# Optimization experiments

Measured on AMD Instinct MI355X. Metric: run time of the kernel, lower is better.

## Reference

```python
import jax, jax.numpy as jnp
import numpy as np

B, S, D, H = 2, 2048, 512, 8
DK = D // H
DECAY = 0.02
LN_EPS = 1e-5


def setup_inputs() -> dict:
    key = jax.random.key(0)
    ks = jax.random.split(key, 16)
    sd = 1.0 / np.sqrt(D)
    def lin(k, fan_in, fan_out):
        return jax.random.uniform(k, (fan_in, fan_out), jnp.float32, -sd, sd)
    return {
        "x": jax.random.normal(ks[0], (B, S, D), jnp.float32),
        "wq": lin(ks[1], D, D), "bq": jnp.zeros((D,), jnp.float32),
        "wk": lin(ks[2], D, D), "bk": jnp.zeros((D,), jnp.float32),
        "wv": lin(ks[3], D, D), "bv": jnp.zeros((D,), jnp.float32),
        "wo": lin(ks[4], D, D), "bo": jnp.zeros((D,), jnp.float32),
        "g1_w": lin(ks[5], D, D // 2), "g1_b": jnp.zeros((D // 2,), jnp.float32),
        "g2_w": lin(ks[6], D // 2, 1), "g2_b": jnp.zeros((1,), jnp.float32),
        "ln_g": jnp.ones((D,), jnp.float32), "ln_b": jnp.zeros((D,), jnp.float32),
    }


def _temporal_bias(seq_len):
    # exp(-decay * |i-j|) masked to lower triangle (causal), additive bias
    pos = jnp.arange(seq_len)
    dist = jnp.abs(pos[:, None] - pos[None, :]).astype(jnp.float32)
    bias = jnp.exp(-DECAY * dist)
    return jnp.tril(bias)  # (S, S)


def reference(x, wq, bq, wk, bk, wv, bv, wo, bo, g1_w, g1_b, g2_w, g2_b, ln_g, ln_b):
    b, s, d = x.shape
    # projections -> (B, H, S, DK)
    q = (x @ wq + bq).reshape(b, s, H, DK).transpose(0, 2, 1, 3)
    k = (x @ wk + bk).reshape(b, s, H, DK).transpose(0, 2, 1, 3)
    v = (x @ wv + bv).reshape(b, s, H, DK).transpose(0, 2, 1, 3)
    scores = jnp.einsum("bhqd,bhkd->bhqk", q, k) / jnp.sqrt(jnp.float32(DK))
    scores = scores + _temporal_bias(s)[None, None, :, :]
    attn = jax.nn.softmax(scores, axis=-1)  # (B, H, S, S)
    out = jnp.einsum("bhqk,bhkd->bhqd", attn, v)
    out = out.transpose(0, 2, 1, 3).reshape(b, s, d)
    out = out @ wo + bo
    # gated residual
    gate = jax.nn.sigmoid(jax.nn.relu(x @ g1_w + g1_b) @ g2_w + g2_b)  # (B, S, 1)
    out = out * gate + x * (1.0 - gate)
    # layer norm
    mu = jnp.mean(out, axis=-1, keepdims=True)
    var = jnp.var(out, axis=-1, keepdims=True)
    y = (out - mu) / jnp.sqrt(var + LN_EPS) * ln_g + ln_b
    return (y, attn)
```

## Files before the change

### kernel.cpp

```cpp
#include <hip/hip_runtime.h>

#define BB 2
#define SS 2048
#define DD 512
#define HH 8
#define DKK 64
#define NROWS (BB * SS)
#define Y_SIZE (BB * SS * DD)

typedef __attribute__((ext_vector_type(8))) short short8;
typedef __attribute__((ext_vector_type(4))) float f32x4;

__device__ __forceinline__ ushort f2bf(float f) {
  union { float f; unsigned u; } v; v.f = f;
  unsigned u = v.u;
  return (ushort)((u + 0x7fffu + ((u >> 16) & 1u)) >> 16);
}


__global__ __launch_bounds__(256) void conv_x_kernel(const float* __restrict__ x,
                                                     ushort* __restrict__ xb) {
  int i = (blockIdx.x * 256 + threadIdx.x) * 4;
  float4 v = *(const float4*)(x + i);
  ushort4 o = {f2bf(v.x), f2bf(v.y), f2bf(v.z), f2bf(v.w)};
  *(ushort4*)(xb + i) = o;
}

__global__ __launch_bounds__(256) void conv_wt_kernel(
    const float* __restrict__ w0, const float* __restrict__ w1,
    const float* __restrict__ w2, const float* __restrict__ w3,
    ushort* __restrict__ o0, ushort* __restrict__ o1,
    ushort* __restrict__ o2, ushort* __restrict__ o3) {
  __shared__ float T[64][65];
  const float* w; ushort* wt;
  switch (blockIdx.z) {
    case 0: w = w0; wt = o0; break;
    case 1: w = w1; wt = o1; break;
    case 2: w = w2; wt = o2; break;
    default: w = w3; wt = o3; break;
  }
  const int t = threadIdx.x;
  const int n0 = blockIdx.x * 64, k0 = blockIdx.y * 64;
#pragma unroll
  for (int i = 0; i < 4; ++i) {
    int c = t + i * 256;
    int row = c >> 4, cc = c & 15;
    float4 v = *(const float4*)(w + (size_t)(k0 + row) * DD + n0 + cc * 4);
    T[row][cc * 4 + 0] = v.x; T[row][cc * 4 + 1] = v.y;
    T[row][cc * 4 + 2] = v.z; T[row][cc * 4 + 3] = v.w;
  }
  __syncthreads();
#pragma unroll
  for (int i = 0; i < 2; ++i) {
    int c = t + i * 256;
    int nr = c >> 3, kc = c & 7;
    ushort4 a, b;
    a.x = f2bf(T[kc * 8 + 0][nr]); a.y = f2bf(T[kc * 8 + 1][nr]);
    a.z = f2bf(T[kc * 8 + 2][nr]); a.w = f2bf(T[kc * 8 + 3][nr]);
    b.x = f2bf(T[kc * 8 + 4][nr]); b.y = f2bf(T[kc * 8 + 5][nr]);
    b.z = f2bf(T[kc * 8 + 6][nr]); b.w = f2bf(T[kc * 8 + 7][nr]);
    *(ushort4*)(wt + (size_t)(n0 + nr) * DD + k0 + kc * 8) = a;
    *(ushort4*)(wt + (size_t)(n0 + nr) * DD + k0 + kc * 8 + 4) = b;
  }
}


__device__ __forceinline__ void mfma_gemm64(
    const ushort* __restrict__ A, int lda, const ushort* __restrict__ B, int ldb,
    int K, ushort (*As)[72], ushort (*Bs)[72], f32x4 (&acc)[2][2], int t) {
  const int l = t & 63, w = t >> 6;
  const int mq = w & 1, nq = w >> 1;
  const int l15 = l & 15, l4 = l >> 4;
  for (int k0 = 0; k0 < K; k0 += 64) {
    __syncthreads();
#pragma unroll
    for (int i = 0; i < 2; ++i) {
      int c = t + i * 256;
      int row = c >> 3, cc = c & 7;
      *(uint4*)&As[row][cc * 8] = *(const uint4*)(A + (size_t)row * lda + k0 + cc * 8);
      *(uint4*)&Bs[row][cc * 8] = *(const uint4*)(B + (size_t)row * ldb + k0 + cc * 8);
    }
    __syncthreads();
    short8 af[2][2], bf[2][2];
#pragma unroll
    for (int mt = 0; mt < 2; ++mt)
#pragma unroll
      for (int ks = 0; ks < 2; ++ks)
        af[mt][ks] = *(const short8*)&As[32 * mq + 16 * mt + l15][ks * 32 + l4 * 8];
#pragma unroll
    for (int nt = 0; nt < 2; ++nt)
#pragma unroll
      for (int ks = 0; ks < 2; ++ks)
        bf[nt][ks] = *(const short8*)&Bs[32 * nq + 16 * nt + l15][ks * 32 + l4 * 8];
#pragma unroll
    for (int mt = 0; mt < 2; ++mt)
#pragma unroll
      for (int nt = 0; nt < 2; ++nt)
#pragma unroll
        for (int ks = 0; ks < 2; ++ks)
          acc[mt][nt] = __builtin_amdgcn_mfma_f32_16x16x32_bf16(
              af[mt][ks], bf[nt][ks], acc[mt][nt], 0, 0, 0);
  }
}


__global__ __launch_bounds__(256) void proj_qkv_kernel(
    const ushort* __restrict__ xb,
    const ushort* __restrict__ wqt, const float* __restrict__ bq,
    const ushort* __restrict__ wkt, const float* __restrict__ bk,
    const ushort* __restrict__ wvt, const float* __restrict__ bv,
    ushort* __restrict__ qb, ushort* __restrict__ kb, ushort* __restrict__ vt) {
  __shared__ ushort As[64][72], Bs[64][72];
  const ushort* W; const float* bias; ushort* out;
  if (blockIdx.z == 0) { W = wqt; bias = bq; out = qb; }
  else if (blockIdx.z == 1) { W = wkt; bias = bk; out = kb; }
  else { W = wvt; bias = bv; out = vt; }
  const int m0 = blockIdx.x * 64;
  const int h = blockIdx.y;
  const int t = threadIdx.x;
  const int l = t & 63, w = t >> 6;
  const int mq = w & 1, nq = w >> 1;
  const int l15 = l & 15, l4 = l >> 4;
  f32x4 acc[2][2] = {};
  mfma_gemm64(xb + (size_t)m0 * DD, DD, W + (size_t)h * DKK * DD, DD, DD,
              As, Bs, acc, t);
  float biasv[2];
#pragma unroll
  for (int nt = 0; nt < 2; ++nt) biasv[nt] = bias[h * DKK + 32 * nq + 16 * nt + l15];

  if (blockIdx.z < 2) {
    __syncthreads();
#pragma unroll
    for (int mt = 0; mt < 2; ++mt)
#pragma unroll
      for (int nt = 0; nt < 2; ++nt)
#pragma unroll
        for (int r = 0; r < 4; ++r)
          As[32 * mq + 16 * mt + l4 * 4 + r][32 * nq + 16 * nt + l15] =
              f2bf(acc[mt][nt][r] + biasv[nt]);
    __syncthreads();
#pragma unroll
    for (int i = 0; i < 2; ++i) {
      int c = t + i * 256;
      int row = c >> 3, cc = c & 7;
      int m = m0 + row, b = m >> 11, s = m & (SS - 1);
      uint4 v = *(const uint4*)&As[row][cc * 8];
      *(uint4*)(out + ((size_t)(b * HH + h) * SS + s) * DKK + cc * 8) = v;
    }
  } else {
#pragma unroll
    for (int mt = 0; mt < 2; ++mt)
#pragma unroll
      for (int nt = 0; nt < 2; ++nt) {
        int dk = 32 * nq + 16 * nt + l15;
        int m = m0 + 32 * mq + 16 * mt + l4 * 4;
        int b = m >> 11, sb = m & (SS - 1);
        ushort4 pk;
        pk.x = f2bf(acc[mt][nt][0] + biasv[nt]);
        pk.y = f2bf(acc[mt][nt][1] + biasv[nt]);
        pk.z = f2bf(acc[mt][nt][2] + biasv[nt]);
        pk.w = f2bf(acc[mt][nt][3] + biasv[nt]);
        *(ushort4*)(out + ((size_t)(b * HH + h) * DKK + dk) * SS + sb) = pk;
      }
  }
}


__global__ __launch_bounds__(256) void attn_kernel(
    const ushort* __restrict__ qb, const ushort* __restrict__ kb,
    const ushort* __restrict__ vt, float* __restrict__ attn,
    ushort* __restrict__ ctx) {
  __shared__ ushort Ks[64][72], Vs[64][72], Ps[64][72];
  __shared__ float rs[64];
  const int t = threadIdx.x;
  const int l = t & 63, w = t >> 6;
  const int mq = w & 1, nq = w >> 1;
  const int l15 = l & 15, l4 = l >> 4;
  const int z = blockIdx.y;
  const int q0 = blockIdx.x * 64;
  if (t < 64) rs[t] = 0.f;

  short8 qf[2][2];
#pragma unroll
  for (int mt = 0; mt < 2; ++mt)
#pragma unroll
    for (int ks = 0; ks < 2; ++ks)
      qf[mt][ks] = *(const short8*)(qb +
          ((size_t)z * SS + q0 + 32 * mq + 16 * mt + l15) * DKK + ks * 32 + l4 * 8);

  float rowf[2][4]; int qi_[2][4];
#pragma unroll
  for (int mt = 0; mt < 2; ++mt)
#pragma unroll
    for (int r = 0; r < 4; ++r) {
      int qi = q0 + 32 * mq + 16 * mt + l4 * 4 + r;
      qi_[mt][r] = qi;
      rowf[mt][r] = __expf(-0.02f * (float)qi);
    }

  float rsp[2][4] = {};
  for (int kt = 0; kt < 32; ++kt) {
    __syncthreads();
#pragma unroll
    for (int i = 0; i < 2; ++i) {
      int c = t + i * 256;
      int row = c >> 3, cc = c & 7;
      *(uint4*)&Ks[row][cc * 8] =
          *(const uint4*)(kb + ((size_t)z * SS + kt * 64 + row) * DKK + cc * 8);
    }
    __syncthreads();
    short8 bf[2][2];
#pragma unroll
    for (int nt = 0; nt < 2; ++nt)
#pragma unroll
      for (int ks = 0; ks < 2; ++ks)
        bf[nt][ks] = *(const short8*)&Ks[32 * nq + 16 * nt + l15][ks * 32 + l4 * 8];
    f32x4 acc[2][2] = {};
#pragma unroll
    for (int mt = 0; mt < 2; ++mt)
#pragma unroll
      for (int nt = 0; nt < 2; ++nt)
#pragma unroll
        for (int ks = 0; ks < 2; ++ks)
          acc[mt][nt] = __builtin_amdgcn_mfma_f32_16x16x32_bf16(
              qf[mt][ks], bf[nt][ks], acc[mt][nt], 0, 0, 0);
#pragma unroll
    for (int nt = 0; nt < 2; ++nt) {
      int kj = kt * 64 + 32 * nq + 16 * nt + l15;
      float colf = __expf(0.02f * (float)kj);
#pragma unroll
      for (int mt = 0; mt < 2; ++mt)
#pragma unroll
        for (int r = 0; r < 4; ++r) {
          float bias = (kj <= qi_[mt][r]) ? rowf[mt][r] * colf : 0.f;
          rsp[mt][r] += __expf(fmaf(acc[mt][nt][r], 0.125f, bias));
        }
    }
  }
#pragma unroll
  for (int mt = 0; mt < 2; ++mt)
#pragma unroll
    for (int r = 0; r < 4; ++r) {
      float v = rsp[mt][r];
      v += __shfl_xor(v, 1); v += __shfl_xor(v, 2);
      v += __shfl_xor(v, 4); v += __shfl_xor(v, 8);
      if (l15 == 0) atomicAdd(&rs[32 * mq + 16 * mt + l4 * 4 + r], v);
    }
  __syncthreads();
  float inv[2][4];
#pragma unroll
  for (int mt = 0; mt < 2; ++mt)
#pragma unroll
    for (int r = 0; r < 4; ++r)
      inv[mt][r] = 1.f / rs[32 * mq + 16 * mt + l4 * 4 + r];

  f32x4 oacc[2][2] = {};
  for (int kt = 0; kt < 32; ++kt) {
    __syncthreads();
#pragma unroll
    for (int i = 0; i < 2; ++i) {
      int c = t + i * 256;
      int row = c >> 3, cc = c & 7;
      *(uint4*)&Ks[row][cc * 8] =
          *(const uint4*)(kb + ((size_t)z * SS + kt * 64 + row) * DKK + cc * 8);
      *(uint4*)&Vs[row][cc * 8] =
          *(const uint4*)(vt + ((size_t)z * DKK + row) * SS + kt * 64 + cc * 8);
    }
    __syncthreads();
    short8 bf[2][2];
#pragma unroll
    for (int nt = 0; nt < 2; ++nt)
#pragma unroll
      for (int ks = 0; ks < 2; ++ks)
        bf[nt][ks] = *(const short8*)&Ks[32 * nq + 16 * nt + l15][ks * 32 + l4 * 8];
    f32x4 acc[2][2] = {};
#pragma unroll
    for (int mt = 0; mt < 2; ++mt)
#pragma unroll
      for (int nt = 0; nt < 2; ++nt)
#pragma unroll
        for (int ks = 0; ks < 2; ++ks)
          acc[mt][nt] = __builtin_amdgcn_mfma_f32_16x16x32_bf16(
              qf[mt][ks], bf[nt][ks], acc[mt][nt], 0, 0, 0);
#pragma unroll
    for (int nt = 0; nt < 2; ++nt) {
      int kj = kt * 64 + 32 * nq + 16 * nt + l15;
      float colf = __expf(0.02f * (float)kj);
#pragma unroll
      for (int mt = 0; mt < 2; ++mt)
#pragma unroll
        for (int r = 0; r < 4; ++r) {
          float bias = (kj <= qi_[mt][r]) ? rowf[mt][r] * colf : 0.f;
          float p = __expf(fmaf(acc[mt][nt][r], 0.125f, bias)) * inv[mt][r];
          attn[((size_t)z * SS + qi_[mt][r]) * SS + kj] = p;
          Ps[32 * mq + 16 * mt + l4 * 4 + r][32 * nq + 16 * nt + l15] = f2bf(p);
        }
    }
    __syncthreads();
    short8 pa[2][2], pb[2][2];
#pragma unroll
    for (int mt = 0; mt < 2; ++mt)
#pragma unroll
      for (int ks = 0; ks < 2; ++ks)
        pa[mt][ks] = *(const short8*)&Ps[32 * mq + 16 * mt + l15][ks * 32 + l4 * 8];
#pragma unroll
    for (int nt = 0; nt < 2; ++nt)
#pragma unroll
      for (int ks = 0; ks < 2; ++ks)
        pb[nt][ks] = *(const short8*)&Vs[32 * nq + 16 * nt + l15][ks * 32 + l4 * 8];
#pragma unroll
    for (int mt = 0; mt < 2; ++mt)
#pragma unroll
      for (int nt = 0; nt < 2; ++nt)
#pragma unroll
        for (int ks = 0; ks < 2; ++ks)
          oacc[mt][nt] = __builtin_amdgcn_mfma_f32_16x16x32_bf16(
              pa[mt][ks], pb[nt][ks], oacc[mt][nt], 0, 0, 0);
  }
  __syncthreads();
#pragma unroll
  for (int mt = 0; mt < 2; ++mt)
#pragma unroll
    for (int nt = 0; nt < 2; ++nt)
#pragma unroll
      for (int r = 0; r < 4; ++r)
        Ps[32 * mq + 16 * mt + l4 * 4 + r][32 * nq + 16 * nt + l15] =
            f2bf(oacc[mt][nt][r]);
  __syncthreads();
  const int b = z >> 3, h = z & 7;
#pragma unroll
  for (int i = 0; i < 2; ++i) {
    int c = t + i * 256;
    int row = c >> 3, cc = c & 7;
    uint4 v = *(const uint4*)&Ps[row][cc * 8];
    *(uint4*)(ctx + ((size_t)(b * SS + q0 + row)) * DD + h * DKK + cc * 8) = v;
  }
}


__global__ __launch_bounds__(256) void proj_o_kernel(
    const ushort* __restrict__ ctx, const ushort* __restrict__ wot,
    const float* __restrict__ bo, float* __restrict__ o) {
  __shared__ ushort As[64][72], Bs[64][72];
  const int m0 = blockIdx.x * 64, n0 = blockIdx.y * 64;
  const int t = threadIdx.x;
  const int l = t & 63, w = t >> 6;
  const int mq = w & 1, nq = w >> 1;
  const int l15 = l & 15, l4 = l >> 4;
  f32x4 acc[2][2] = {};
  mfma_gemm64(ctx + (size_t)m0 * DD, DD, wot + (size_t)n0 * DD, DD, DD,
              As, Bs, acc, t);
#pragma unroll
  for (int nt = 0; nt < 2; ++nt) {
    int col = n0 + 32 * nq + 16 * nt + l15;
    float bv = bo[col];
#pragma unroll
    for (int mt = 0; mt < 2; ++mt)
#pragma unroll
      for (int r = 0; r < 4; ++r) {
        int m = m0 + 32 * mq + 16 * mt + l4 * 4 + r;
        o[(size_t)m * DD + col] = acc[mt][nt][r] + bv;
      }
  }
}


__global__ __launch_bounds__(256) void gate_kernel(
    const float* __restrict__ x, const float* __restrict__ g1w,
    const float* __restrict__ g1b, const float* __restrict__ g2w,
    const float* __restrict__ g2b, float* __restrict__ gate) {
  __shared__ float xs[8][512];
  __shared__ float red[32];
  const int r0 = blockIdx.x * 8;
  const int t = threadIdx.x;
  const float4* xg = (const float4*)&x[(size_t)r0 * DD];
  float4* xsv = (float4*)&xs[0][0];
#pragma unroll
  for (int i = 0; i < 4; ++i) xsv[t + i * 256] = xg[t + i * 256];
  __syncthreads();
  float acc[8] = {};
  for (int i = 0; i < 512; i += 4) {
    float w0 = g1w[(i + 0) * 256 + t];
    float w1 = g1w[(i + 1) * 256 + t];
    float w2 = g1w[(i + 2) * 256 + t];
    float w3 = g1w[(i + 3) * 256 + t];
#pragma unroll
    for (int r = 0; r < 8; ++r) {
      float4 xv = *(const float4*)&xs[r][i];
      acc[r] += xv.x * w0 + xv.y * w1 + xv.z * w2 + xv.w * w3;
    }
  }
  float b1 = g1b[t], w2_ = g2w[t];
  float p[8];
#pragma unroll
  for (int r = 0; r < 8; ++r) {
    float h = acc[r] + b1;
    h = h > 0.f ? h : 0.f;
    p[r] = h * w2_;
  }
#pragma unroll
  for (int r = 0; r < 8; ++r)
    for (int off = 32; off; off >>= 1) p[r] += __shfl_xor(p[r], off, 64);
  if ((t & 63) == 0) {
#pragma unroll
    for (int r = 0; r < 8; ++r) red[r * 4 + (t >> 6)] = p[r];
  }
  __syncthreads();
  if (t < 8) {
    float s = red[t * 4] + red[t * 4 + 1] + red[t * 4 + 2] + red[t * 4 + 3] + g2b[0];
    gate[r0 + t] = 1.f / (1.f + __expf(-s));
  }
}


__global__ __launch_bounds__(256) void blend_ln_kernel(
    const float* __restrict__ o, const float* __restrict__ x,
    const float* __restrict__ gate, const float* __restrict__ ln_g,
    const float* __restrict__ ln_b, float* __restrict__ y) {
  __shared__ float r1[4], r2[4];
  const int row = blockIdx.x, t = threadIdx.x;
  float g = gate[row];
  float2 o2 = *(const float2*)&o[(size_t)row * DD + t * 2];
  float2 x2 = *(const float2*)&x[(size_t)row * DD + t * 2];
  float va = o2.x * g + x2.x * (1.f - g);
  float vb = o2.y * g + x2.y * (1.f - g);
  float s = va + vb, q = va * va + vb * vb;
  for (int off = 32; off; off >>= 1) {
    s += __shfl_xor(s, off, 64);
    q += __shfl_xor(q, off, 64);
  }
  if ((t & 63) == 0) { r1[t >> 6] = s; r2[t >> 6] = q; }
  __syncthreads();
  s = r1[0] + r1[1] + r1[2] + r1[3];
  q = r2[0] + r2[1] + r2[2] + r2[3];
  float mean = s * (1.f / 512.f);
  float var = q * (1.f / 512.f) - mean * mean;
  float rstd = rsqrtf(var + 1e-5f);
  float2 lg = *(const float2*)&ln_g[t * 2];
  float2 lb = *(const float2*)&ln_b[t * 2];
  float2 out;
  out.x = (va - mean) * rstd * lg.x + lb.x;
  out.y = (vb - mean) * rstd * lg.y + lb.y;
  *(float2*)&y[(size_t)row * DD + t * 2] = out;
}

extern "C" void kernel_launch(void* const* d_in, const int* in_sizes, int n_in,
                              void* d_out, int out_size, void* d_ws, size_t ws_size,
                              hipStream_t stream) {
  const float* x   = (const float*)d_in[0];
  const float* wq  = (const float*)d_in[1];
  const float* bq  = (const float*)d_in[2];
  const float* wk  = (const float*)d_in[3];
  const float* bk  = (const float*)d_in[4];
  const float* wv  = (const float*)d_in[5];
  const float* bv  = (const float*)d_in[6];
  const float* wo  = (const float*)d_in[7];
  const float* bo  = (const float*)d_in[8];
  const float* g1w = (const float*)d_in[9];
  const float* g1b = (const float*)d_in[10];
  const float* g2w = (const float*)d_in[11];
  const float* g2b = (const float*)d_in[12];
  const float* lng = (const float*)d_in[13];
  const float* lnb = (const float*)d_in[14];

  float* y    = (float*)d_out;
  float* attn = y + (size_t)Y_SIZE;

  char* ws = (char*)d_ws;
  ushort* xb  = (ushort*)(ws);
  ushort* wqt = (ushort*)(ws + (4 << 20));
  ushort* wkt = (ushort*)(ws + (4 << 20) + (512 << 10));
  ushort* wvt = (ushort*)(ws + (5 << 20));
  ushort* wot = (ushort*)(ws + (5 << 20) + (512 << 10));
  ushort* qb  = (ushort*)(ws + (6 << 20));
  ushort* kb  = (ushort*)(ws + (10 << 20));
  ushort* vt  = (ushort*)(ws + (14 << 20));
  ushort* ctx = (ushort*)(ws + (18 << 20));
  float*  o   = (float*)(ws + (22 << 20));
  float*  gate= (float*)(ws + (30 << 20));

  hipLaunchKernelGGL(conv_x_kernel, dim3(Y_SIZE / 1024), dim3(256), 0, stream, x, xb);
  hipLaunchKernelGGL(conv_wt_kernel, dim3(8, 8, 4), dim3(256), 0, stream,
                     wq, wk, wv, wo, wqt, wkt, wvt, wot);
  hipLaunchKernelGGL(proj_qkv_kernel, dim3(64, 8, 3), dim3(256), 0, stream,
                     xb, wqt, bq, wkt, bk, wvt, bv, qb, kb, vt);
  hipLaunchKernelGGL(gate_kernel, dim3(512), dim3(256), 0, stream,
                     x, g1w, g1b, g2w, g2b, gate);
  hipLaunchKernelGGL(attn_kernel, dim3(32, 16), dim3(256), 0, stream,
                     qb, kb, vt, attn, ctx);
  hipLaunchKernelGGL(proj_o_kernel, dim3(64, 8), dim3(256), 0, stream,
                     ctx, wot, bo, o);
  hipLaunchKernelGGL(blend_ln_kernel, dim3(4096), dim3(256), 0, stream,
                     o, x, gate, lng, lnb, y);
}
```

Before: 446.3 us.

## Double-buffer attention tiles via register prefetch with 512-thread blocks

Rewrites the attention kernel to use 512-thread blocks that process 128-key tiles. The next K/V tile is prefetched into registers while the current tile is computed, which is meant to hide global-load latency behind MFMA and softmax work. It also raises wave priority around the MFMA blocks, uses explicit barriers and waitcnt in place of __syncthreads, and swaps the grid order so blocks of the same head are adjacent. In exchange it increases register pressure and LDS footprint and needs careful manual synchronisation.

```diff
diff --git a/kernel.cpp b/kernel.cpp
--- a/kernel.cpp
+++ b/kernel.cpp
@@ -166,18 +166,26 @@
 }
 
 
-__global__ __launch_bounds__(256) void attn_kernel(
+#define LGKM0() do { asm volatile("s_waitcnt lgkmcnt(0)" ::: "memory"); \
+                     __builtin_amdgcn_sched_barrier(0); } while (0)
+#define BARRIER() do { __builtin_amdgcn_sched_barrier(0); \
+                       __builtin_amdgcn_s_barrier(); \
+                       __builtin_amdgcn_sched_barrier(0); } while (0)
+
+__global__ __launch_bounds__(512, 2) void attn_kernel(
     const ushort* __restrict__ qb, const ushort* __restrict__ kb,
     const ushort* __restrict__ vt, float* __restrict__ attn,
     ushort* __restrict__ ctx) {
-  __shared__ ushort Ks[64][72], Vs[64][72], Ps[64][72];
+  __shared__ __align__(16) ushort Ks[128][72];
+  __shared__ __align__(16) ushort Vs[64][136];
+  __shared__ __align__(16) ushort Ps[64][136];
   __shared__ float rs[64];
   const int t = threadIdx.x;
   const int l = t & 63, w = t >> 6;
   const int mq = w & 1, nq = w >> 1;
   const int l15 = l & 15, l4 = l >> 4;
-  const int z = blockIdx.y;
-  const int q0 = blockIdx.x * 64;
+  const int z = blockIdx.x;
+  const int q0 = blockIdx.y * 64;
   if (t < 64) rs[t] = 0.f;
 
   short8 qf[2][2];
@@ -198,24 +206,46 @@
       rowf[mt][r] = __expf(-0.02f * (float)qi);
     }
 
+  uint4 kr[2], vr[2];
+  const int krow = t >> 3, kcol = (t & 7) * 8;
+  const int krow2 = krow + 64;
+  const int vrow = t >> 4, vcol = (t & 15) * 8;
+  const int vrow2 = vrow + 32;
+
+  auto kload = [&](int kt2) {
+    const ushort* p = kb + ((size_t)z * SS + (size_t)kt2 * 128) * DKK;
+    kr[0] = *(const uint4*)(p + (size_t)krow * DKK + kcol);
+    kr[1] = *(const uint4*)(p + (size_t)krow2 * DKK + kcol);
+  };
+  auto vload = [&](int kt2) {
+    const ushort* p = vt + (size_t)z * DKK * SS + kt2 * 128;
+    vr[0] = *(const uint4*)(p + (size_t)vrow * SS + vcol);
+    vr[1] = *(const uint4*)(p + (size_t)vrow2 * SS + vcol);
+  };
+  auto kwrite = [&]() {
+    *(uint4*)&Ks[krow][kcol] = kr[0];
+    *(uint4*)&Ks[krow2][kcol] = kr[1];
+  };
+  auto vwrite = [&]() {
+    *(uint4*)&Vs[vrow][vcol] = vr[0];
+    *(uint4*)&Vs[vrow2][vcol] = vr[1];
+  };
+
+  kload(0);
+  kwrite();
+  LGKM0(); BARRIER();
+
   float rsp[2][4] = {};
-  for (int kt = 0; kt < 32; ++kt) {
-    __syncthreads();
-#pragma unroll
-    for (int i = 0; i < 2; ++i) {
-      int c = t + i * 256;
-      int row = c >> 3, cc = c & 7;
-      *(uint4*)&Ks[row][cc * 8] =
-          *(const uint4*)(kb + ((size_t)z * SS + kt * 64 + row) * DKK + cc * 8);
-    }
-    __syncthreads();
-    short8 bf[2][2];
+  for (int kt = 0; kt < 16; ++kt) {
+    if (kt < 15) kload(kt + 1);
+    short8 bfr[2][2];
 #pragma unroll
     for (int nt = 0; nt < 2; ++nt)
 #pragma unroll
       for (int ks = 0; ks < 2; ++ks)
-        bf[nt][ks] = *(const short8*)&Ks[32 * nq + 16 * nt + l15][ks * 32 + l4 * 8];
+        bfr[nt][ks] = *(const short8*)&Ks[32 * nq + 16 * nt + l15][ks * 32 + l4 * 8];
     f32x4 acc[2][2] = {};
+    __builtin_amdgcn_s_setprio(1);
 #pragma unroll
     for (int mt = 0; mt < 2; ++mt)
 #pragma unroll
@@ -223,10 +253,11 @@
 #pragma unroll
         for (int ks = 0; ks < 2; ++ks)
           acc[mt][nt] = __builtin_amdgcn_mfma_f32_16x16x32_bf16(
-              qf[mt][ks], bf[nt][ks], acc[mt][nt], 0, 0, 0);
+              qf[mt][ks], bfr[nt][ks], acc[mt][nt], 0, 0, 0);
+    __builtin_amdgcn_s_setprio(0);
 #pragma unroll
     for (int nt = 0; nt < 2; ++nt) {
-      int kj = kt * 64 + 32 * nq + 16 * nt + l15;
+      int kj = kt * 128 + 32 * nq + 16 * nt + l15;
       float colf = __expf(0.02f * (float)kj);
 #pragma unroll
       for (int mt = 0; mt < 2; ++mt)
@@ -236,7 +267,12 @@
           rsp[mt][r] += __expf(fmaf(acc[mt][nt][r], 0.125f, bias));
         }
     }
-  }
+    BARRIER();
+    if (kt < 15) { kwrite(); LGKM0(); BARRIER(); }
+  }
+
+  kload(0); vload(0);
+
 #pragma unroll
   for (int mt = 0; mt < 2; ++mt)
 #pragma unroll
@@ -253,27 +289,20 @@
 #pragma unroll
     for (int r = 0; r < 4; ++r)
       inv[mt][r] = 1.f / rs[32 * mq + 16 * mt + l4 * 4 + r];
-
-  f32x4 oacc[2][2] = {};
-  for (int kt = 0; kt < 32; ++kt) {
-    __syncthreads();
-#pragma unroll
-    for (int i = 0; i < 2; ++i) {
-      int c = t + i * 256;
-      int row = c >> 3, cc = c & 7;
-      *(uint4*)&Ks[row][cc * 8] =
-          *(const uint4*)(kb + ((size_t)z * SS + kt * 64 + row) * DKK + cc * 8);
-      *(uint4*)&Vs[row][cc * 8] =
-          *(const uint4*)(vt + ((size_t)z * DKK + row) * SS + kt * 64 + cc * 8);
-    }
-    __syncthreads();
-    short8 bf[2][2];
+  kwrite(); vwrite();
+  LGKM0(); BARRIER();
+
+  f32x4 oacc[2] = {};
+  for (int kt = 0; kt < 16; ++kt) {
+    if (kt < 15) { kload(kt + 1); vload(kt + 1); }
+    short8 bfr[2][2];
 #pragma unroll
     for (int nt = 0; nt < 2; ++nt)
 #pragma unroll
       for (int ks = 0; ks < 2; ++ks)
-        bf[nt][ks] = *(const short8*)&Ks[32 * nq + 16 * nt + l15][ks * 32 + l4 * 8];
+        bfr[nt][ks] = *(const short8*)&Ks[32 * nq + 16 * nt + l15][ks * 32 + l4 * 8];
     f32x4 acc[2][2] = {};
+    __builtin_amdgcn_s_setprio(1);
 #pragma unroll
     for (int mt = 0; mt < 2; ++mt)
 #pragma unroll
@@ -281,10 +310,11 @@
 #pragma unroll
         for (int ks = 0; ks < 2; ++ks)
           acc[mt][nt] = __builtin_amdgcn_mfma_f32_16x16x32_bf16(
-              qf[mt][ks], bf[nt][ks], acc[mt][nt], 0, 0, 0);
+              qf[mt][ks], bfr[nt][ks], acc[mt][nt], 0, 0, 0);
+    __builtin_amdgcn_s_setprio(0);
 #pragma unroll
     for (int nt = 0; nt < 2; ++nt) {
-      int kj = kt * 64 + 32 * nq + 16 * nt + l15;
+      int kj = kt * 128 + 32 * nq + 16 * nt + l15;
       float colf = __expf(0.02f * (float)kj);
 #pragma unroll
       for (int mt = 0; mt < 2; ++mt)
@@ -296,44 +326,33 @@
           Ps[32 * mq + 16 * mt + l4 * 4 + r][32 * nq + 16 * nt + l15] = f2bf(p);
         }
     }
-    __syncthreads();
-    short8 pa[2][2], pb[2][2];
-#pragma unroll
-    for (int mt = 0; mt < 2; ++mt)
-#pragma unroll
-      for (int ks = 0; ks < 2; ++ks)
-        pa[mt][ks] = *(const short8*)&Ps[32 * mq + 16 * mt + l15][ks * 32 + l4 * 8];
-#pragma unroll
-    for (int nt = 0; nt < 2; ++nt)
-#pragma unroll
-      for (int ks = 0; ks < 2; ++ks)
-        pb[nt][ks] = *(const short8*)&Vs[32 * nq + 16 * nt + l15][ks * 32 + l4 * 8];
-#pragma unroll
-    for (int mt = 0; mt < 2; ++mt)
-#pragma unroll
-      for (int nt = 0; nt < 2; ++nt)
-#pragma unroll
-        for (int ks = 0; ks < 2; ++ks)
-          oacc[mt][nt] = __builtin_amdgcn_mfma_f32_16x16x32_bf16(
-              pa[mt][ks], pb[nt][ks], oacc[mt][nt], 0, 0, 0);
-  }
-  __syncthreads();
+    LGKM0(); BARRIER();
+    __builtin_amdgcn_s_setprio(1);
+#pragma unroll
+    for (int ks = 0; ks < 4; ++ks) {
+      short8 pb = *(const short8*)&Vs[16 * nq + l15][ks * 32 + l4 * 8];
+#pragma unroll
+      for (int mt = 0; mt < 2; ++mt) {
+        short8 pa = *(const short8*)&Ps[32 * mq + 16 * mt + l15][ks * 32 + l4 * 8];
+        oacc[mt] = __builtin_amdgcn_mfma_f32_16x16x32_bf16(pa, pb, oacc[mt], 0, 0, 0);
+      }
+    }
+    __builtin_amdgcn_s_setprio(0);
+    BARRIER();
+    if (kt < 15) { kwrite(); vwrite(); LGKM0(); BARRIER(); }
+  }
+
 #pragma unroll
   for (int mt = 0; mt < 2; ++mt)
 #pragma unroll
-    for (int nt = 0; nt < 2; ++nt)
-#pragma unroll
-      for (int r = 0; r < 4; ++r)
-        Ps[32 * mq + 16 * mt + l4 * 4 + r][32 * nq + 16 * nt + l15] =
-            f2bf(oacc[mt][nt][r]);
-  __syncthreads();
-  const int b = z >> 3, h = z & 7;
-#pragma unroll
-  for (int i = 0; i < 2; ++i) {
-    int c = t + i * 256;
-    int row = c >> 3, cc = c & 7;
-    uint4 v = *(const uint4*)&Ps[row][cc * 8];
-    *(uint4*)(ctx + ((size_t)(b * SS + q0 + row)) * DD + h * DKK + cc * 8) = v;
+    for (int r = 0; r < 4; ++r)
+      Ps[32 * mq + 16 * mt + l4 * 4 + r][16 * nq + l15] = f2bf(oacc[mt][r]);
+  LGKM0(); BARRIER();
+  {
+    const int b = z >> 3, h = z & 7;
+    const int row = t >> 3, cc = t & 7;
+    *(uint4*)(ctx + ((size_t)(b * SS + q0 + row)) * DD + h * DKK + cc * 8) =
+        *(const uint4*)&Ps[row][cc * 8];
   }
 }
 
@@ -486,7 +505,7 @@
                      xb, wqt, bq, wkt, bk, wvt, bv, qb, kb, vt);
   hipLaunchKernelGGL(gate_kernel, dim3(512), dim3(256), 0, stream,
                      x, g1w, g1b, g2w, g2b, gate);
-  hipLaunchKernelGGL(attn_kernel, dim3(32, 16), dim3(256), 0, stream,
+  hipLaunchKernelGGL(attn_kernel, dim3(16, 32), dim3(512), 0, stream,
                      qb, kb, vt, attn, ctx);
   hipLaunchKernelGGL(proj_o_kernel, dim3(64, 8), dim3(256), 0, stream,
                      ctx, wot, bo, o);
```

Result: slower. 495.9 us (+11.1%).

## Single-pass attention with deferred normalization and separate attn-scaling kernel

Applied to the files above, without the earlier changes.

Drops the first QK^T pass that only computed row sums. Unnormalized exp scores are written out, and the sums are gathered in the same loop. Each row is then rescaled in a separate kernel, optionally from a bf16 staging buffer. The 1/8 score scale is folded into the Q projection, and the S tile is computed transposed so each thread can vectorize its stores. No max subtraction is used, so this relies on small scores. The bf16 staging path loses precision in the stored attn matrix and adds an extra read and write of the full attention matrix.

```diff
diff --git a/kernel.cpp b/kernel.cpp
--- a/kernel.cpp
+++ b/kernel.cpp
@@ -15,6 +15,11 @@
   union { float f; unsigned u; } v; v.f = f;
   unsigned u = v.u;
   return (ushort)((u + 0x7fffu + ((u >> 16) & 1u)) >> 16);
+}
+
+__device__ __forceinline__ float bf2f(ushort u) {
+  union { unsigned u; float f; } v; v.u = ((unsigned)u) << 16;
+  return v.f;
 }
 
 
@@ -115,6 +120,7 @@
   if (blockIdx.z == 0) { W = wqt; bias = bq; out = qb; }
   else if (blockIdx.z == 1) { W = wkt; bias = bk; out = kb; }
   else { W = wvt; bias = bv; out = vt; }
+  const float scale = (blockIdx.z == 0) ? 0.125f : 1.0f;
   const int m0 = blockIdx.x * 64;
   const int h = blockIdx.y;
   const int t = threadIdx.x;
@@ -137,7 +143,7 @@
 #pragma unroll
         for (int r = 0; r < 4; ++r)
           As[32 * mq + 16 * mt + l4 * 4 + r][32 * nq + 16 * nt + l15] =
-              f2bf(acc[mt][nt][r] + biasv[nt]);
+              f2bf((acc[mt][nt][r] + biasv[nt]) * scale);
     __syncthreads();
 #pragma unroll
     for (int i = 0; i < 2; ++i) {
@@ -166,95 +172,40 @@
 }
 
 
+template <int BF16P>
 __global__ __launch_bounds__(256) void attn_kernel(
     const ushort* __restrict__ qb, const ushort* __restrict__ kb,
-    const ushort* __restrict__ vt, float* __restrict__ attn,
-    ushort* __restrict__ ctx) {
+    const ushort* __restrict__ vt, void* __restrict__ pout,
+    float* __restrict__ invb, ushort* __restrict__ ctx) {
   __shared__ ushort Ks[64][72], Vs[64][72], Ps[64][72];
   __shared__ float rs[64];
   const int t = threadIdx.x;
   const int l = t & 63, w = t >> 6;
   const int mq = w & 1, nq = w >> 1;
   const int l15 = l & 15, l4 = l >> 4;
-  const int z = blockIdx.y;
-  const int q0 = blockIdx.x * 64;
+  const int z = blockIdx.x;
+  const int q0 = blockIdx.y * 64;
   if (t < 64) rs[t] = 0.f;
 
   short8 qf[2][2];
 #pragma unroll
-  for (int mt = 0; mt < 2; ++mt)
+  for (int bt = 0; bt < 2; ++bt)
 #pragma unroll
     for (int ks = 0; ks < 2; ++ks)
-      qf[mt][ks] = *(const short8*)(qb +
-          ((size_t)z * SS + q0 + 32 * mq + 16 * mt + l15) * DKK + ks * 32 + l4 * 8);
-
-  float rowf[2][4]; int qi_[2][4];
-#pragma unroll
-  for (int mt = 0; mt < 2; ++mt)
-#pragma unroll
-    for (int r = 0; r < 4; ++r) {
-      int qi = q0 + 32 * mq + 16 * mt + l4 * 4 + r;
-      qi_[mt][r] = qi;
-      rowf[mt][r] = __expf(-0.02f * (float)qi);
-    }
-
-  float rsp[2][4] = {};
-  for (int kt = 0; kt < 32; ++kt) {
-    __syncthreads();
-#pragma unroll
-    for (int i = 0; i < 2; ++i) {
-      int c = t + i * 256;
-      int row = c >> 3, cc = c & 7;
-      *(uint4*)&Ks[row][cc * 8] =
-          *(const uint4*)(kb + ((size_t)z * SS + kt * 64 + row) * DKK + cc * 8);
-    }
-    __syncthreads();
-    short8 bf[2][2];
-#pragma unroll
-    for (int nt = 0; nt < 2; ++nt)
-#pragma unroll
-      for (int ks = 0; ks < 2; ++ks)
-        bf[nt][ks] = *(const short8*)&Ks[32 * nq + 16 * nt + l15][ks * 32 + l4 * 8];
-    f32x4 acc[2][2] = {};
-#pragma unroll
-    for (int mt = 0; mt < 2; ++mt)
-#pragma unroll
-      for (int nt = 0; nt < 2; ++nt)
-#pragma unroll
-        for (int ks = 0; ks < 2; ++ks)
-          acc[mt][nt] = __builtin_amdgcn_mfma_f32_16x16x32_bf16(
-              qf[mt][ks], bf[nt][ks], acc[mt][nt], 0, 0, 0);
-#pragma unroll
-    for (int nt = 0; nt < 2; ++nt) {
-      int kj = kt * 64 + 32 * nq + 16 * nt + l15;
-      float colf = __expf(0.02f * (float)kj);
-#pragma unroll
-      for (int mt = 0; mt < 2; ++mt)
-#pragma unroll
-        for (int r = 0; r < 4; ++r) {
-          float bias = (kj <= qi_[mt][r]) ? rowf[mt][r] * colf : 0.f;
-          rsp[mt][r] += __expf(fmaf(acc[mt][nt][r], 0.125f, bias));
-        }
-    }
-  }
-#pragma unroll
-  for (int mt = 0; mt < 2; ++mt)
-#pragma unroll
-    for (int r = 0; r < 4; ++r) {
-      float v = rsp[mt][r];
-      v += __shfl_xor(v, 1); v += __shfl_xor(v, 2);
-      v += __shfl_xor(v, 4); v += __shfl_xor(v, 8);
-      if (l15 == 0) atomicAdd(&rs[32 * mq + 16 * mt + l4 * 4 + r], v);
-    }
-  __syncthreads();
-  float inv[2][4];
-#pragma unroll
-  for (int mt = 0; mt < 2; ++mt)
-#pragma unroll
-    for (int r = 0; r < 4; ++r)
-      inv[mt][r] = 1.f / rs[32 * mq + 16 * mt + l4 * 4 + r];
-
+      qf[bt][ks] = *(const short8*)(qb +
+          ((size_t)z * SS + q0 + 32 * mq + 16 * bt + l15) * DKK + ks * 32 + l4 * 8);
+
+  int qi_[2]; float rowf[2];
+#pragma unroll
+  for (int bt = 0; bt < 2; ++bt) {
+    qi_[bt] = q0 + 32 * mq + 16 * bt + l15;
+    rowf[bt] = __expf(-0.02f * (float)qi_[bt]);
+  }
+  const float c_r[4] = {1.0f, 1.0202013f, 1.0408108f, 1.0618365f};
+
+  float rsp[2] = {0.f, 0.f};
   f32x4 oacc[2][2] = {};
+
   for (int kt = 0; kt < 32; ++kt) {
     __syncthreads();
 #pragma unroll
@@ -267,34 +218,48 @@
           *(const uint4*)(vt + ((size_t)z * DKK + row) * SS + kt * 64 + cc * 8);
     }
     __syncthreads();
-    short8 bf[2][2];
-#pragma unroll
-    for (int nt = 0; nt < 2; ++nt)
+    short8 kf[2][2];
+#pragma unroll
+    for (int at = 0; at < 2; ++at)
 #pragma unroll
       for (int ks = 0; ks < 2; ++ks)
-        bf[nt][ks] = *(const short8*)&Ks[32 * nq + 16 * nt + l15][ks * 32 + l4 * 8];
+        kf[at][ks] = *(const short8*)&Ks[32 * nq + 16 * at + l15][ks * 32 + l4 * 8];
     f32x4 acc[2][2] = {};
 #pragma unroll
-    for (int mt = 0; mt < 2; ++mt)
-#pragma unroll
-      for (int nt = 0; nt < 2; ++nt)
+    for (int at = 0; at < 2; ++at)
+#pragma unroll
+      for (int bt = 0; bt < 2; ++bt)
 #pragma unroll
         for (int ks = 0; ks < 2; ++ks)
-          acc[mt][nt] = __builtin_amdgcn_mfma_f32_16x16x32_bf16(
-              qf[mt][ks], bf[nt][ks], acc[mt][nt], 0, 0, 0);
-#pragma unroll
-    for (int nt = 0; nt < 2; ++nt) {
-      int kj = kt * 64 + 32 * nq + 16 * nt + l15;
-      float colf = __expf(0.02f * (float)kj);
-#pragma unroll
-      for (int mt = 0; mt < 2; ++mt)
+          acc[at][bt] = __builtin_amdgcn_mfma_f32_16x16x32_bf16(
+              kf[at][ks], qf[bt][ks], acc[at][bt], 0, 0, 0);
+#pragma unroll
+    for (int at = 0; at < 2; ++at) {
+      const int kjbase = kt * 64 + 32 * nq + 16 * at + l4 * 4;
+      const float colb = __expf(0.02f * (float)kjbase);
+#pragma unroll
+      for (int bt = 0; bt < 2; ++bt) {
+        const float rc = rowf[bt] * colb;
+        ushort4 us;
+        float pv[4];
 #pragma unroll
         for (int r = 0; r < 4; ++r) {
-          float bias = (kj <= qi_[mt][r]) ? rowf[mt][r] * colf : 0.f;
-          float p = __expf(fmaf(acc[mt][nt][r], 0.125f, bias)) * inv[mt][r];
-          attn[((size_t)z * SS + qi_[mt][r]) * SS + kj] = p;
-          Ps[32 * mq + 16 * mt + l4 * 4 + r][32 * nq + 16 * nt + l15] = f2bf(p);
+          float bias = (kjbase + r <= qi_[bt]) ? rc * c_r[r] : 0.f;
+          float p = __expf(acc[at][bt][r] + bias);
+          pv[r] = p;
+          rsp[bt] += p;
         }
+        us.x = f2bf(pv[0]); us.y = f2bf(pv[1]);
+        us.z = f2bf(pv[2]); us.w = f2bf(pv[3]);
+        *(ushort4*)&Ps[32 * mq + 16 * bt + l15][32 * nq + 16 * at + l4 * 4] = us;
+        const size_t gidx = ((size_t)z * SS + qi_[bt]) * SS + kjbase;
+        if (BF16P) {
+          *(ushort4*)((ushort*)pout + gidx) = us;
+        } else {
+          float4 f4 = {pv[0], pv[1], pv[2], pv[3]};
+          *(float4*)((float*)pout + gidx) = f4;
+        }
+      }
     }
     __syncthreads();
     short8 pa[2][2], pb[2][2];
@@ -317,7 +282,23 @@
           oacc[mt][nt] = __builtin_amdgcn_mfma_f32_16x16x32_bf16(
               pa[mt][ks], pb[nt][ks], oacc[mt][nt], 0, 0, 0);
   }
+
+#pragma unroll
+  for (int bt = 0; bt < 2; ++bt) {
+    float v = rsp[bt];
+    v += __shfl_xor(v, 16);
+    v += __shfl_xor(v, 32);
+    if (l < 16) atomicAdd(&rs[32 * mq + 16 * bt + l], v);
+  }
   __syncthreads();
+  if (t < 64) invb[(size_t)z * SS + q0 + t] = 1.f / rs[t];
+  float invr[2][4];
+#pragma unroll
+  for (int mt = 0; mt < 2; ++mt)
+#pragma unroll
+    for (int r = 0; r < 4; ++r)
+      invr[mt][r] = 1.f / rs[32 * mq + 16 * mt + l4 * 4 + r];
+
 #pragma unroll
   for (int mt = 0; mt < 2; ++mt)
 #pragma unroll
@@ -325,7 +306,7 @@
 #pragma unroll
       for (int r = 0; r < 4; ++r)
         Ps[32 * mq + 16 * mt + l4 * 4 + r][32 * nq + 16 * nt + l15] =
-            f2bf(oacc[mt][nt][r]);
+            f2bf(oacc[mt][nt][r] * invr[mt][r]);
   __syncthreads();
   const int b = z >> 3, h = z & 7;
 #pragma unroll
@@ -335,6 +316,39 @@
     uint4 v = *(const uint4*)&Ps[row][cc * 8];
     *(uint4*)(ctx + ((size_t)(b * SS + q0 + row)) * DD + h * DKK + cc * 8) = v;
   }
+}
+
+
+__global__ __launch_bounds__(256) void scale_attn_bf(
+    const ushort* __restrict__ pbuf, const float* __restrict__ invb,
+    float* __restrict__ attn) {
+  const size_t row = blockIdx.x;
+  const float inv = invb[row];
+  const int t = threadIdx.x;
+  const size_t base = row * SS + t * 8;
+  uint4 u = *(const uint4*)(pbuf + base);
+  const ushort* us = (const ushort*)&u;
+  float4 a, b;
+  a.x = bf2f(us[0]) * inv; a.y = bf2f(us[1]) * inv;
+  a.z = bf2f(us[2]) * inv; a.w = bf2f(us[3]) * inv;
+  b.x = bf2f(us[4]) * inv; b.y = bf2f(us[5]) * inv;
+  b.z = bf2f(us[6]) * inv; b.w = bf2f(us[7]) * inv;
+  *(float4*)(attn + base) = a;
+  *(float4*)(attn + base + 4) = b;
+}
+
+__global__ __launch_bounds__(256) void scale_attn_f32(
+    float* __restrict__ attn, const float* __restrict__ invb) {
+  const size_t row = blockIdx.x;
+  const float inv = invb[row];
+  const int t = threadIdx.x;
+  const size_t base = row * SS + t * 8;
+  float4 a = *(const float4*)(attn + base);
+  float4 b = *(const float4*)(attn + base + 4);
+  a.x *= inv; a.y *= inv; a.z *= inv; a.w *= inv;
+  b.x *= inv; b.y *= inv; b.z *= inv; b.w *= inv;
+  *(float4*)(attn + base) = a;
+  *(float4*)(attn + base + 4) = b;
 }
 
 
@@ -478,6 +492,10 @@
   ushort* ctx = (ushort*)(ws + (18 << 20));
   float*  o   = (float*)(ws + (22 << 20));
   float*  gate= (float*)(ws + (30 << 20));
+  float*  invb= (float*)(ws + (30 << 20) + (256 << 10));
+  ushort* pbuf= (ushort*)(ws + (32 << 20));
+
+  const bool bigws = ws_size >= ((size_t)168 << 20);
 
   hipLaunchKernelGGL(conv_x_kernel, dim3(Y_SIZE / 1024), dim3(256), 0, stream, x, xb);
   hipLaunchKernelGGL(conv_wt_kernel, dim3(8, 8, 4), dim3(256), 0, stream,
@@ -486,8 +504,17 @@
                      xb, wqt, bq, wkt, bk, wvt, bv, qb, kb, vt);
   hipLaunchKernelGGL(gate_kernel, dim3(512), dim3(256), 0, stream,
                      x, g1w, g1b, g2w, g2b, gate);
-  hipLaunchKernelGGL(attn_kernel, dim3(32, 16), dim3(256), 0, stream,
-                     qb, kb, vt, attn, ctx);
+  if (bigws) {
+    hipLaunchKernelGGL(attn_kernel<1>, dim3(16, 32), dim3(256), 0, stream,
+                       qb, kb, vt, (void*)pbuf, invb, ctx);
+    hipLaunchKernelGGL(scale_attn_bf, dim3(BB * HH * SS), dim3(256), 0, stream,
+                       pbuf, invb, attn);
+  } else {
+    hipLaunchKernelGGL(attn_kernel<0>, dim3(16, 32), dim3(256), 0, stream,
+                       qb, kb, vt, (void*)attn, invb, ctx);
+    hipLaunchKernelGGL(scale_attn_f32, dim3(BB * HH * SS), dim3(256), 0, stream,
+                       attn, invb);
+  }
   hipLaunchKernelGGL(proj_o_kernel, dim3(64, 8), dim3(256), 0, stream,
                      ctx, wot, bo, o);
   hipLaunchKernelGGL(blend_ln_kernel, dim3(4096), dim3(256), 0, stream,
```

After: 484.7 us. +8.6%, slower.
